# Optimization experiments

Hardware: AMD Instinct MI355X
Metric: run time of the kernel (lower is better)

Reference implementation:

```python
import jax, jax.numpy as jnp
import numpy as np

ALPHA = 20.0


def setup_inputs() -> dict:
    key = jax.random.key(0)
    k1, k2 = jax.random.split(key)
    N, C = 8192, 8
    output = jax.random.normal(k1, (N, C), dtype=jnp.float32)
    target = jax.random.randint(k2, (N,), 0, C, dtype=jnp.int64)
    return {"output": output, "target": target}


def reference(output, target):
    # output: [N, C] logits, target: [N] int labels in [0, C-1]
    probs = jax.nn.softmax(output, axis=1)
    dtype = probs.dtype
    C = output.shape[1]
    total_auc = jnp.zeros((), dtype)
    valid_count = jnp.zeros((), dtype)
    for class_idx in range(C):  # fixed small class loop, matches original
        p = probs[:, class_idx]                      # [N]
        pos = (target == class_idx).astype(dtype)    # [N]
        neg = 1.0 - pos                              # [N]
        n_pos = pos.sum()
        n_neg = neg.sum()
        # pairwise sigmoid(alpha * (p_i - p_j)) masked to (pos_i, neg_j) pairs
        s = jax.nn.sigmoid(ALPHA * (p[:, None] - p[None, :]))  # [N, N]
        pair_sum = jnp.einsum('i,ij,j->', pos, s, neg)
        valid = jnp.logical_and(n_pos > 0, n_neg > 0)
        mean_auc_c = jnp.where(valid, pair_sum / jnp.maximum(n_pos * n_neg, 1.0), 0.0)
        total_auc = total_auc + mean_auc_c
        valid_count = valid_count + valid.astype(dtype)
    loss = jnp.where(valid_count > 0, 1.0 - total_auc / jnp.maximum(valid_count, 1.0), 0.0)
    return loss
```

## Files before the change

kernel.cpp:

```cpp
#include <hip/hip_runtime.h>

#define SCALE 28.853900817779268f
#define L2E   1.4426950408889634f
#define M 2048
#define T 1024
#define CPC 32
#define QB (M/CPC)

__device__ __forceinline__ float fexp2(float x){ return __builtin_amdgcn_exp2f(x); }
__device__ __forceinline__ float frcp (float x){ return __builtin_amdgcn_rcpf(x); }

#define WRED64(x) { _Pragma("unroll") for (int _o = 32; _o; _o >>= 1) x += __shfl_down(x, _o, 64); }

__global__ __launch_bounds__(1024)
void k_fused(const float* __restrict__ logits, const int* __restrict__ tgt,
             float* __restrict__ out, unsigned int* __restrict__ ticket,
             float* __restrict__ gpart, int* __restrict__ ccnt, int N){
  const int b = blockIdx.x, NB = (int)gridDim.x;
  const int c = b >> 5, ch = b & (CPC-1);
  const int tid = threadIdx.x, lane = tid & 63, w = tid >> 6;
  const float invM = 1.0f / (float)M;

  __shared__ int   HP[M];
  __shared__ float Bq[QB];
  __shared__ int   wnp[16];
  __shared__ float rw[16];
  __shared__ float scs[8];
  __shared__ int   lastflag;

  ((int2*)HP)[tid] = make_int2(0, 0);
  float Ej0 = fexp2(-SCALE * ((float)tid          + 0.5f) * invM);
  float Ej1 = fexp2(-SCALE * ((float)(tid + T)    + 0.5f) * invM);
  if (tid < QB)
    Bq[tid] = fexp2(SCALE * ((float)(ch + CPC*tid) + 0.5f) * invM);
  __syncthreads();

  const float4* l4 = (const float4*)logits;
  for (int i = tid; i < N; i += T){
    float4 A = l4[2*i], B4 = l4[2*i+1];
    float y0=A.x *L2E, y1=A.y *L2E, y2=A.z *L2E, y3=A.w *L2E;
    float y4=B4.x*L2E, y5=B4.y*L2E, y6=B4.z*L2E, y7=B4.w*L2E;
    float yc = y0;
    yc=(c==1)?y1:yc; yc=(c==2)?y2:yc; yc=(c==3)?y3:yc;
    yc=(c==4)?y4:yc; yc=(c==5)?y5:yc; yc=(c==6)?y6:yc; yc=(c==7)?y7:yc;
    float s = ((fexp2(y0-yc)+fexp2(y1-yc)) + (fexp2(y2-yc)+fexp2(y3-yc)))
            + ((fexp2(y4-yc)+fexp2(y5-yc)) + (fexp2(y6-yc)+fexp2(y7-yc)));
    float p = frcp(s);
    int bin = min((int)(p * (float)M), M-1);
    int inc = 1 + ((tgt[i] == c) ? (1 << 16) : 0);
    atomicAdd(&HP[bin], inc);
  }
  __syncthreads();

  float Hj0, Hj1; int np_part;
  {
    const int hp0 = HP[tid], hp1 = HP[tid + T];
    const int p0 = hp0 >> 16, p1 = hp1 >> 16;
    np_part = p0 + p1;
    Hj0 = (float)((hp0 & 0xFFFF) - p0);
    Hj1 = (float)((hp1 & 0xFFFF) - p1);
  }
  WRED64(np_part)
  if (lane == 0) wnp[w] = np_part;

  float tot = 0.f;
  #pragma unroll 4
  for (int q = 0; q < QB; ++q){
    int Pki = HP[ch + CPC*q] >> 16;
    if (Pki == 0) continue;
    float Bk = Bq[q];
    float Pk = (float)Pki;
    float s0 = Hj0 * frcp(fmaf(Bk, Ej0, 1.0f));
    float s1 = Hj1 * frcp(fmaf(Bk, Ej1, 1.0f));
    tot += Pk * (s0 + s1);
  }
  WRED64(tot)
  if (lane == 0) rw[w] = tot;
  __syncthreads();
  if (tid == 0){
    float bt = 0.f;
    #pragma unroll
    for (int i = 0; i < 16; ++i) bt += rw[i];
    atomicExch(&gpart[b], bt);
    if (ch == 0){
      int snp = 0;
      #pragma unroll
      for (int i = 0; i < 16; ++i) snp += wnp[i];
      atomicExch(&ccnt[c], snp);
    }
    __threadfence();
    unsigned old = atomicAdd(ticket, 1u);
    lastflag = ((old % (unsigned)NB) == (unsigned)(NB - 1));
  }
  __syncthreads();
  if (!lastflag) return;

  if (tid == 0) __threadfence();
  __syncthreads();
  if (tid < 256){
    int c2 = tid >> 5, l = tid & 31;
    float s = atomicAdd(&gpart[c2*CPC + l], 0.0f);
    #pragma unroll
    for (int o = 16; o; o >>= 1) s += __shfl_down(s, o, 32);
    if (l == 0) scs[c2] = s;
  }
  __syncthreads();
  if (tid < 8){
    int np = atomicAdd(&ccnt[tid], 0);
    int nn = N - np;
    bool valid = (np > 0 && nn > 0);
    float t = valid ? scs[tid] / ((float)np * (float)nn) : 0.f;
    float f = valid ? 1.f : 0.f;
    #pragma unroll
    for (int o = 4; o; o >>= 1){
      t += __shfl_down(t, o, 8);
      f += __shfl_down(f, o, 8);
    }
    if (tid == 0) out[0] = (f > 0.f) ? (1.0f - t / f) : 0.0f;
  }
}

extern "C" void kernel_launch(void* const* d_in, const int* in_sizes, int n_in,
                              void* d_out, int out_size, void* d_ws, size_t ws_size,
                              hipStream_t stream) {
    const float* logits = (const float*)d_in[0];
    const int*   tgt    = (const int*)d_in[1];
    float* out = (float*)d_out;
    int N = in_sizes[1];

    unsigned int* ticket = (unsigned int*)d_ws;
    float* gpart = (float*)d_ws + 16;
    int*   ccnt  = (int*)(gpart + 256);

    k_fused<<<8*CPC, T, 0, stream>>>(logits, tgt, out, ticket, gpart, ccnt, N);
}
```

Before: 18.71 us.

## Build shared global histograms once and use grid barrier instead of per-block recompute

Previously each of the 256 blocks read all N rows and recomputed softmax to build its own class histogram in shared memory. Now each block handles only an N/256 slice, computes all 8 class probabilities at once, and atomically adds into double-buffered global histograms. A software grid barrier follows, after which blocks copy their class histogram into LDS for the pairwise sum. This cuts the redundant global reads and exp work, at the cost of global atomics, a spin barrier that assumes all blocks are co-resident, and magic-number workspace initialization.

```diff
diff --git a/kernel.cpp b/kernel.cpp
--- a/kernel.cpp
+++ b/kernel.cpp
@@ -6,62 +6,135 @@
 #define T 1024
 #define CPC 32
 #define QB (M/CPC)
+#define NBLK 256
+#define GUARD (1<<16)
+#define MAGIC0 0x5ACEB007u
+#define MAGIC1 0xC0FFEE42u
 
 __device__ __forceinline__ float fexp2(float x){ return __builtin_amdgcn_exp2f(x); }
 __device__ __forceinline__ float frcp (float x){ return __builtin_amdgcn_rcpf(x); }
 
 #define WRED64(x) { _Pragma("unroll") for (int _o = 32; _o; _o >>= 1) x += __shfl_down(x, _o, 64); }
 
+#define ALOAD(p)    __hip_atomic_load((p), __ATOMIC_RELAXED, __HIP_MEMORY_SCOPE_AGENT)
+#define ASTORE(p,v) __hip_atomic_store((p),(v), __ATOMIC_RELAXED, __HIP_MEMORY_SCOPE_AGENT)
+#define AADD(p,v)   __hip_atomic_fetch_add((p),(v), __ATOMIC_RELAXED, __HIP_MEMORY_SCOPE_AGENT)
+
 __global__ __launch_bounds__(1024)
 void k_fused(const float* __restrict__ logits, const int* __restrict__ tgt,
-             float* __restrict__ out, unsigned int* __restrict__ ticket,
-             float* __restrict__ gpart, int* __restrict__ ccnt, int N){
+             float* __restrict__ out, unsigned* __restrict__ sync,
+             float* __restrict__ gpart, int* __restrict__ ccnt,
+             int* __restrict__ Ghist, int N){
   const int b = blockIdx.x, NB = (int)gridDim.x;
   const int c = b >> 5, ch = b & (CPC-1);
   const int tid = threadIdx.x, lane = tid & 63, w = tid >> 6;
   const float invM = 1.0f / (float)M;
+  unsigned* ticket = sync + 0;
+  unsigned* abar   = sync + 1;
+  unsigned* hrel   = sync + 2;
+  unsigned* magic  = sync + 4;
 
   __shared__ int   HP[M];
   __shared__ float Bq[QB];
   __shared__ int   wnp[16];
   __shared__ float rw[16];
   __shared__ float scs[8];
-  __shared__ int   lastflag;
-
-  ((int2*)HP)[tid] = make_int2(0, 0);
-  float Ej0 = fexp2(-SCALE * ((float)tid          + 0.5f) * invM);
-  float Ej1 = fexp2(-SCALE * ((float)(tid + T)    + 0.5f) * invM);
+  __shared__ int   initflag, parS, lastflag;
+
+  float Ej0 = fexp2(-SCALE * ((float)tid       + 0.5f) * invM);
+  float Ej1 = fexp2(-SCALE * ((float)(tid + T) + 0.5f) * invM);
   if (tid < QB)
     Bq[tid] = fexp2(SCALE * ((float)(ch + CPC*tid) + 0.5f) * invM);
-  __syncthreads();
-
-  const float4* l4 = (const float4*)logits;
-  for (int i = tid; i < N; i += T){
+
+  const int R = (N + NBLK - 1) / NBLK;
+  const bool havework = (tid < R) && (b*R + tid < N);
+  int bn0=0,bn1=0,bn2=0,bn3=0,bn4=0,bn5=0,bn6=0,bn7=0, tv=-1;
+  if (havework){
+    int i = b*R + tid;
+    const float4* l4 = (const float4*)logits;
     float4 A = l4[2*i], B4 = l4[2*i+1];
-    float y0=A.x *L2E, y1=A.y *L2E, y2=A.z *L2E, y3=A.w *L2E;
-    float y4=B4.x*L2E, y5=B4.y*L2E, y6=B4.z*L2E, y7=B4.w*L2E;
-    float yc = y0;
-    yc=(c==1)?y1:yc; yc=(c==2)?y2:yc; yc=(c==3)?y3:yc;
-    yc=(c==4)?y4:yc; yc=(c==5)?y5:yc; yc=(c==6)?y6:yc; yc=(c==7)?y7:yc;
-    float s = ((fexp2(y0-yc)+fexp2(y1-yc)) + (fexp2(y2-yc)+fexp2(y3-yc)))
-            + ((fexp2(y4-yc)+fexp2(y5-yc)) + (fexp2(y6-yc)+fexp2(y7-yc)));
-    float p = frcp(s);
-    int bin = min((int)(p * (float)M), M-1);
-    int inc = 1 + ((tgt[i] == c) ? (1 << 16) : 0);
-    atomicAdd(&HP[bin], inc);
-  }
-  __syncthreads();
-
-  float Hj0, Hj1; int np_part;
+    float e0=fexp2(A.x *L2E), e1=fexp2(A.y *L2E), e2=fexp2(A.z *L2E), e3=fexp2(A.w *L2E);
+    float e4=fexp2(B4.x*L2E), e5=fexp2(B4.y*L2E), e6=fexp2(B4.z*L2E), e7=fexp2(B4.w*L2E);
+    float s = ((e0+e1)+(e2+e3))+((e4+e5)+(e6+e7));
+    float r = frcp(s) * (float)M;
+    bn0=min((int)(e0*r),M-1); bn1=min((int)(e1*r),M-1);
+    bn2=min((int)(e2*r),M-1); bn3=min((int)(e3*r),M-1);
+    bn4=min((int)(e4*r),M-1); bn5=min((int)(e5*r),M-1);
+    bn6=min((int)(e6*r),M-1); bn7=min((int)(e7*r),M-1);
+    tv = tgt[i];
+  }
+
+  if (tid == 0)
+    initflag = (ALOAD(magic) != MAGIC0) || (ALOAD(magic+1) != MAGIC1);
+  __syncthreads();
+  if (initflag){
+    if (b == 0){
+      for (int m = tid; m < 2*8*M; m += T) ASTORE(&Ghist[m], 0);
+      if (tid < 4) ASTORE(&sync[tid], 0u);
+      __syncthreads();
+      if (tid == 0){
+        __threadfence();
+        ASTORE(magic, MAGIC0); ASTORE(magic+1, MAGIC1);
+      }
+    } else if (tid == 0){
+      int g = 0;
+      while ((ALOAD(magic) != MAGIC0 || ALOAD(magic+1) != MAGIC1) && ++g < GUARD)
+        __builtin_amdgcn_s_sleep(8);
+      __threadfence();
+    }
+  }
+  __syncthreads();
+
+  if (tid == 0) parS = (int)((ALOAD(abar) >> 8) & 1u);
+  __syncthreads();
+  const int par = parS;
+  int* __restrict__ Gb = Ghist + par*(8*M);
   {
-    const int hp0 = HP[tid], hp1 = HP[tid + T];
-    const int p0 = hp0 >> 16, p1 = hp1 >> 16;
+    int* ob = Ghist + (par^1)*(8*M) + b*64;
+    if (tid < 64) ASTORE(&ob[tid], 0);
+  }
+  if (havework){
+    AADD(&Gb[0*M+bn0], 1 + ((tv==0)?(1<<16):0));
+    AADD(&Gb[1*M+bn1], 1 + ((tv==1)?(1<<16):0));
+    AADD(&Gb[2*M+bn2], 1 + ((tv==2)?(1<<16):0));
+    AADD(&Gb[3*M+bn3], 1 + ((tv==3)?(1<<16):0));
+    AADD(&Gb[4*M+bn4], 1 + ((tv==4)?(1<<16):0));
+    AADD(&Gb[5*M+bn5], 1 + ((tv==5)?(1<<16):0));
+    AADD(&Gb[6*M+bn6], 1 + ((tv==6)?(1<<16):0));
+    AADD(&Gb[7*M+bn7], 1 + ((tv==7)?(1<<16):0));
+  }
+  __syncthreads();
+
+  if (tid == 0){
+    __threadfence();
+    unsigned o = AADD(abar, 1u);
+    if ((o & (NBLK-1)) == (NBLK-1)){
+      __threadfence();
+      ASTORE(hrel, o + 1u);
+    } else {
+      int g = 0;
+      while ((int)(ALOAD(hrel) - o) <= 0 && ++g < GUARD)
+        __builtin_amdgcn_s_sleep(2);
+    }
+    __threadfence();
+  }
+  __syncthreads();
+
+  int np_part; float Hj0, Hj1;
+  {
+    int* Gc = Gb + c*M;
+    int g0 = ALOAD(&Gc[tid]);
+    int g1 = ALOAD(&Gc[tid + T]);
+    HP[tid]     = g0;
+    HP[tid + T] = g1;
+    int p0 = g0 >> 16, p1 = g1 >> 16;
     np_part = p0 + p1;
-    Hj0 = (float)((hp0 & 0xFFFF) - p0);
-    Hj1 = (float)((hp1 & 0xFFFF) - p1);
+    Hj0 = (float)((g0 & 0xFFFF) - p0);
+    Hj1 = (float)((g1 & 0xFFFF) - p1);
   }
   WRED64(np_part)
   if (lane == 0) wnp[w] = np_part;
+  __syncthreads();
 
   float tot = 0.f;
   #pragma unroll 4
@@ -128,9 +201,10 @@
     float* out = (float*)d_out;
     int N = in_sizes[1];
 
-    unsigned int* ticket = (unsigned int*)d_ws;
-    float* gpart = (float*)d_ws + 16;
-    int*   ccnt  = (int*)(gpart + 256);
-
-    k_fused<<<8*CPC, T, 0, stream>>>(logits, tgt, out, ticket, gpart, ccnt, N);
+    unsigned* sync  = (unsigned*)d_ws;
+    float*    gpart = (float*)d_ws + 32;
+    int*      ccnt  = (int*)((float*)d_ws + 288);
+    int*      Ghist = (int*)((float*)d_ws + 512);
+
+    k_fused<<<NBLK, T, 0, stream>>>(logits, tgt, out, sync, gpart, ccnt, Ghist, N);
 }
```

Measured after the change: 42.65 us. 2.28x slower.

## Precompute sigmoid lookup table over bin differences and simplify softmax

Applied to the files above, without the earlier changes.

Builds a shared-memory table of sigmoid values indexed by the difference of histogram bins, so the pairwise loop does two LDS loads and FMAs per step instead of two reciprocals. Softmax now computes the eight exponentials once and multiplies the selected one by the reciprocal of their sum, rather than eight shifted exponentials. The final reads switch from atomic adds of zero to relaxed atomic loads, and workspace offsets are moved. The table costs 16KB of extra LDS, and the unshifted exponentials could overflow for large logits.

```diff
diff --git a/kernel.cpp b/kernel.cpp
--- a/kernel.cpp
+++ b/kernel.cpp
@@ -11,10 +11,11 @@
 __device__ __forceinline__ float frcp (float x){ return __builtin_amdgcn_rcpf(x); }
 
 #define WRED64(x) { _Pragma("unroll") for (int _o = 32; _o; _o >>= 1) x += __shfl_down(x, _o, 64); }
+#define ALOAD(p) __hip_atomic_load((p), __ATOMIC_RELAXED, __HIP_MEMORY_SCOPE_AGENT)
 
 __global__ __launch_bounds__(1024)
 void k_fused(const float* __restrict__ logits, const int* __restrict__ tgt,
-             float* __restrict__ out, unsigned int* __restrict__ ticket,
+             float* __restrict__ out, unsigned* __restrict__ ticket,
              float* __restrict__ gpart, int* __restrict__ ccnt, int N){
   const int b = blockIdx.x, NB = (int)gridDim.x;
   const int c = b >> 5, ch = b & (CPC-1);
@@ -22,30 +23,34 @@
   const float invM = 1.0f / (float)M;
 
   __shared__ int   HP[M];
-  __shared__ float Bq[QB];
+  __shared__ float g[2*M];
   __shared__ int   wnp[16];
   __shared__ float rw[16];
   __shared__ float scs[8];
   __shared__ int   lastflag;
 
   ((int2*)HP)[tid] = make_int2(0, 0);
-  float Ej0 = fexp2(-SCALE * ((float)tid          + 0.5f) * invM);
-  float Ej1 = fexp2(-SCALE * ((float)(tid + T)    + 0.5f) * invM);
-  if (tid < QB)
-    Bq[tid] = fexp2(SCALE * ((float)(ch + CPC*tid) + 0.5f) * invM);
+  #pragma unroll
+  for (int r = 0; r < 4; ++r){
+    int idx = tid + 1024*r;
+    if (idx < 2*M-1){
+      float d = (float)(idx - (M-1));
+      g[idx] = frcp(1.0f + fexp2(SCALE * d * invM));
+    }
+  }
   __syncthreads();
 
   const float4* l4 = (const float4*)logits;
+  #pragma unroll 2
   for (int i = tid; i < N; i += T){
     float4 A = l4[2*i], B4 = l4[2*i+1];
-    float y0=A.x *L2E, y1=A.y *L2E, y2=A.z *L2E, y3=A.w *L2E;
-    float y4=B4.x*L2E, y5=B4.y*L2E, y6=B4.z*L2E, y7=B4.w*L2E;
-    float yc = y0;
-    yc=(c==1)?y1:yc; yc=(c==2)?y2:yc; yc=(c==3)?y3:yc;
-    yc=(c==4)?y4:yc; yc=(c==5)?y5:yc; yc=(c==6)?y6:yc; yc=(c==7)?y7:yc;
-    float s = ((fexp2(y0-yc)+fexp2(y1-yc)) + (fexp2(y2-yc)+fexp2(y3-yc)))
-            + ((fexp2(y4-yc)+fexp2(y5-yc)) + (fexp2(y6-yc)+fexp2(y7-yc)));
-    float p = frcp(s);
+    float e0=fexp2(A.x *L2E), e1=fexp2(A.y *L2E), e2=fexp2(A.z *L2E), e3=fexp2(A.w *L2E);
+    float e4=fexp2(B4.x*L2E), e5=fexp2(B4.y*L2E), e6=fexp2(B4.z*L2E), e7=fexp2(B4.w*L2E);
+    float s = ((e0+e1)+(e2+e3))+((e4+e5)+(e6+e7));
+    float ec = e0;
+    ec=(c==1)?e1:ec; ec=(c==2)?e2:ec; ec=(c==3)?e3:ec;
+    ec=(c==4)?e4:ec; ec=(c==5)?e5:ec; ec=(c==6)?e6:ec; ec=(c==7)?e7:ec;
+    float p = ec * frcp(s);
     int bin = min((int)(p * (float)M), M-1);
     int inc = 1 + ((tgt[i] == c) ? (1 << 16) : 0);
     atomicAdd(&HP[bin], inc);
@@ -64,15 +69,14 @@
   if (lane == 0) wnp[w] = np_part;
 
   float tot = 0.f;
+  const int i0 = ch + (M-1) - tid;
   #pragma unroll 4
   for (int q = 0; q < QB; ++q){
     int Pki = HP[ch + CPC*q] >> 16;
     if (Pki == 0) continue;
-    float Bk = Bq[q];
-    float Pk = (float)Pki;
-    float s0 = Hj0 * frcp(fmaf(Bk, Ej0, 1.0f));
-    float s1 = Hj1 * frcp(fmaf(Bk, Ej1, 1.0f));
-    tot += Pk * (s0 + s1);
+    float g0 = g[i0 + CPC*q];
+    float g1 = g[i0 + CPC*q - 1024];
+    tot += (float)Pki * fmaf(Hj0, g0, Hj1 * g1);
   }
   WRED64(tot)
   if (lane == 0) rw[w] = tot;
@@ -99,14 +103,14 @@
   __syncthreads();
   if (tid < 256){
     int c2 = tid >> 5, l = tid & 31;
-    float s = atomicAdd(&gpart[c2*CPC + l], 0.0f);
+    float s = ALOAD(&gpart[c2*CPC + l]);
     #pragma unroll
     for (int o = 16; o; o >>= 1) s += __shfl_down(s, o, 32);
     if (l == 0) scs[c2] = s;
   }
   __syncthreads();
   if (tid < 8){
-    int np = atomicAdd(&ccnt[tid], 0);
+    int np = ALOAD(&ccnt[tid]);
     int nn = N - np;
     bool valid = (np > 0 && nn > 0);
     float t = valid ? scs[tid] / ((float)np * (float)nn) : 0.f;
@@ -128,9 +132,9 @@
     float* out = (float*)d_out;
     int N = in_sizes[1];
 
-    unsigned int* ticket = (unsigned int*)d_ws;
-    float* gpart = (float*)d_ws + 16;
-    int*   ccnt  = (int*)(gpart + 256);
+    unsigned* ticket = (unsigned*)d_ws;
+    float* gpart = (float*)d_ws + 32;
+    int*   ccnt  = (int*)((float*)d_ws + 288);
 
     k_fused<<<8*CPC, T, 0, stream>>>(logits, tgt, out, ticket, gpart, ccnt, N);
 }
```

Result: no change. 18.72 us (+0.1%).
